# Kernel optimization log

Measured on AMD Instinct MI355X. Metric: run time of the kernel, lower is better.

## Reference

```python
import jax, jax.numpy as jnp
import numpy as np

SCALE = 2
GROUPS = 4

def _up_axis(x, axis, s):
    # torch F.interpolate bilinear, align_corners=False, along one axis
    n = x.shape[axis]
    src = jnp.maximum((jnp.arange(n * s, dtype=jnp.float32) + 0.5) / s - 0.5, 0.0)
    i0 = jnp.minimum(jnp.floor(src).astype(jnp.int32), n - 1)
    i1 = jnp.minimum(i0 + 1, n - 1)
    t = (src - i0.astype(jnp.float32)).astype(x.dtype)
    shp = [1] * x.ndim
    shp[axis] = -1
    t = t.reshape(shp)
    return jnp.take(x, i0, axis=axis) * (1 - t) + jnp.take(x, i1, axis=axis) * t

def _grid_sample(img, grid):
    # img: (N,C,H,W); grid: (N,Hg,Wg,2) xy in [-1,1]; bilinear, align_corners=False, zeros padding
    N, C, H, W = img.shape
    gx = (grid[..., 0] + 1.0) * (W * 0.5) - 0.5
    gy = (grid[..., 1] + 1.0) * (H * 0.5) - 0.5
    x0 = jnp.floor(gx)
    y0 = jnp.floor(gy)
    tx = (gx - x0).astype(img.dtype)
    ty = (gy - y0).astype(img.dtype)
    x0 = x0.astype(jnp.int32)
    y0 = y0.astype(jnp.int32)
    flat = img.reshape(N, C, H * W)

    def corner(xi, yi, wgt):
        valid = ((xi >= 0) & (xi < W) & (yi >= 0) & (yi < H)).astype(img.dtype)
        idx = (jnp.clip(yi, 0, H - 1) * W + jnp.clip(xi, 0, W - 1)).reshape(N, -1)
        v = jax.vmap(lambda f, i: f[:, i])(flat, idx)  # (N,C,P) irregular gather
        return v * (wgt * valid).reshape(N, 1, -1)

    out = (corner(x0, y0, (1 - tx) * (1 - ty))
           + corner(x0 + 1, y0, tx * (1 - ty))
           + corner(x0, y0 + 1, (1 - tx) * ty)
           + corner(x0 + 1, y0 + 1, tx * ty))
    return out.reshape(N, C, grid.shape[1], grid.shape[2])

def _forward(x, w_off, b_off, w_mask, b_mask):
    s, g = SCALE, GROUPS
    b, c, h, w = x.shape
    # 1x1 convs
    offset = jnp.einsum('bchw,oc->bohw', x, w_off) + b_off[None, :, None, None]  # (b,2g,h,w)
    mask = jax.nn.sigmoid(jnp.einsum('bchw,gc->bghw', x, w_mask) + b_mask[None, :, None, None])  # (b,g,h,w)
    # bilinear upsample then split into s*s subpixel feature maps (one per group)
    x_up = _up_axis(_up_axis(x, 2, s), 3, s)  # (b,c,s*h,s*w)
    feat = x_up.reshape(b, c, s, h, s, w).transpose(0, 2, 4, 1, 3, 5).reshape(b, s * s, c, h, w)[:, :g]
    # per-group offset-perturbed sampling coordinates
    off = offset.reshape(b, g, 2, h, w).transpose(0, 1, 3, 4, 2)  # (b,g,h,w,2) (x,y)
    gy, gx = jnp.meshgrid(jnp.arange(h, dtype=x.dtype), jnp.arange(w, dtype=x.dtype), indexing='ij')
    base = jnp.stack([gx, gy], axis=-1)  # (h,w,2)
    coords = base[None, None] + off
    norm = (coords / jnp.array([w, h], dtype=x.dtype) - 0.5) * 2.0
    sampled = _grid_sample(feat.reshape(b * g, c, h, w), norm.reshape(b * g, h, w, 2))
    sampled = sampled.reshape(b, g, c, h, w)
    # sigmoid-mask weighting and group-sum reduction
    return (sampled * mask[:, :, None]).sum(axis=1)  # (b,c,h,w)

def setup_inputs():
    key = jax.random.key(0)
    k1, k2, k3, k4, k5 = jax.random.split(key, 5)
    b, c, h, w, g = 16, 64, 128, 128, GROUPS
    return {
        'x': jax.random.normal(k1, (b, c, h, w), jnp.float32),
        'w_off': jax.random.normal(k2, (2 * g, c), jnp.float32) * 0.1,
        'b_off': jax.random.normal(k3, (2 * g,), jnp.float32) * 0.1,
        'w_mask': jax.random.normal(k4, (g, c), jnp.float32) * 0.1,
        'b_mask': jax.random.normal(k5, (g,), jnp.float32) * 0.1,
    }

def reference(x, w_off, b_off, w_mask, b_mask):
    return _forward(x, w_off, b_off, w_mask, b_mask)
```

## Files before the change

kernel.cpp:

```cpp
#include <hip/hip_runtime.h>
#include <hip/hip_fp16.h>

#define CC 64
#define HH 128
#define WW 128
#define HWS (HH * WW)
#define NG 4

__device__ __forceinline__ void make_taps(float gp, int n, int half, int& base,
                                          float& w0o, float& w1o, float& w2o) {
  float w0 = 0.0f, w1 = 0.0f, w2 = 0.0f;
  float f = floorf(gp);
  int x0 = (int)f;
  float t = gp - f;
  int b = 0;
#pragma unroll
  for (int k = 0; k < 2; ++k) {
    int xc = x0 + k;
    float cw = k ? t : 1.0f - t;
    if (xc < 0 || xc >= n) cw = 0.0f;
    int xcc = min(max(xc, 0), n - 1);
    int u = half * n + xcc;
    float src = fmaxf((float)u * 0.5f - 0.25f, 0.0f);
    float sf = floorf(src);
    int i0 = (int)sf;
    float tu = src - sf;
    int i1 = min(i0 + 1, n - 1);
    if (k == 0) b = i0;
    int s0 = i0 - b;
    int s1 = i1 - b;
    float a0 = cw * (1.0f - tu);
    float a1 = cw * tu;
    w0 += (s0 == 0) ? a0 : 0.0f;
    w1 += (s0 == 1) ? a0 : 0.0f;
    w0 += (s1 == 0) ? a1 : 0.0f;
    w1 += (s1 == 1) ? a1 : 0.0f;
    w2 += (s1 == 2) ? a1 : 0.0f;
  }
  base = b;
  w0o = w0; w1o = w1; w2o = w2;
}

__global__ __launch_bounds__(256) void prep_v3(
    const float* __restrict__ x,
    const float* __restrict__ w_off, const float* __restrict__ b_off,
    const float* __restrict__ w_mask, const float* __restrict__ b_mask,
    __half* __restrict__ xT, float* __restrict__ geomC, int npix) {
  __shared__ float wt[CC * 12];
  __shared__ unsigned int tile[64][33];
  __shared__ float part[4][64][13];
  int t = threadIdx.x;
  for (int idx = t; idx < CC * 12; idx += 256) {
    int c = idx / 12, d = idx - c * 12;
    wt[idx] = (d < 8) ? w_off[d * CC + c] : w_mask[(d - 8) * CC + c];
  }
  __syncthreads();

  int px = t & 63, chq = t >> 6;
  int pix = blockIdx.x * 64 + px;
  int b = pix >> 14;
  int ij = pix & (HWS - 1);
  const float* __restrict__ xp = x + (size_t)b * CC * HWS + ij;

  float xv[16];
#pragma unroll
  for (int k = 0; k < 16; ++k) xv[k] = xp[(size_t)(chq * 16 + k) * HWS];

  float p12[12];
#pragma unroll
  for (int d = 0; d < 12; ++d) p12[d] = 0.0f;
#pragma unroll
  for (int k = 0; k < 16; ++k) {
    int c = chq * 16 + k;
    float v = xv[k];
    const float4 w0 = *reinterpret_cast<const float4*>(&wt[c * 12 + 0]);
    const float4 w1 = *reinterpret_cast<const float4*>(&wt[c * 12 + 4]);
    const float4 w2 = *reinterpret_cast<const float4*>(&wt[c * 12 + 8]);
    p12[0]  = fmaf(w0.x, v, p12[0]);   p12[1]  = fmaf(w0.y, v, p12[1]);
    p12[2]  = fmaf(w0.z, v, p12[2]);   p12[3]  = fmaf(w0.w, v, p12[3]);
    p12[4]  = fmaf(w1.x, v, p12[4]);   p12[5]  = fmaf(w1.y, v, p12[5]);
    p12[6]  = fmaf(w1.z, v, p12[6]);   p12[7]  = fmaf(w1.w, v, p12[7]);
    p12[8]  = fmaf(w2.x, v, p12[8]);   p12[9]  = fmaf(w2.y, v, p12[9]);
    p12[10] = fmaf(w2.z, v, p12[10]);  p12[11] = fmaf(w2.w, v, p12[11]);
  }

#pragma unroll
  for (int k = 0; k < 8; ++k) {
    tile[px][chq * 8 + k] = __builtin_bit_cast(
        unsigned int, __floats2half2_rn(xv[2 * k], xv[2 * k + 1]));
  }
#pragma unroll
  for (int d = 0; d < 12; ++d) part[chq][px][d] = p12[d];
  __syncthreads();

  {
    unsigned int* __restrict__ xtu = reinterpret_cast<unsigned int*>(xT);
    size_t base = (size_t)blockIdx.x * 64 * 32;
    int spx = t >> 2, c0 = (t & 3) * 8;
    uint4 u0, u1;
    u0.x = tile[spx][c0 + 0]; u0.y = tile[spx][c0 + 1];
    u0.z = tile[spx][c0 + 2]; u0.w = tile[spx][c0 + 3];
    u1.x = tile[spx][c0 + 4]; u1.y = tile[spx][c0 + 5];
    u1.z = tile[spx][c0 + 6]; u1.w = tile[spx][c0 + 7];
    *reinterpret_cast<uint4*>(xtu + base + t * 8) = u0;
    *reinterpret_cast<uint4*>(xtu + base + t * 8 + 4) = u1;
  }

  if (t < 64) {
    int pixg = blockIdx.x * 64 + t;
    int ijg = pixg & (HWS - 1);
    int i = ijg >> 7, j = ijg & (WW - 1);
    float a12[12];
#pragma unroll
    for (int d = 0; d < 12; ++d) {
      a12[d] = ((d < 8) ? b_off[d] : b_mask[d - 8]) + part[0][t][d] +
               part[1][t][d] + part[2][t][d] + part[3][t][d];
    }
    float* __restrict__ gb = geomC + (size_t)(pixg >> 5) * 1024 + (pixg & 31);
#pragma unroll
    for (int g = 0; g < NG; ++g) {
      int sy = g >> 1, sx = g & 1;
      float mg = 1.0f / (1.0f + __expf(-a12[8 + g]));
      int cb, rb;
      float x0, x1, x2, y0, y1, y2;
      make_taps((float)j + a12[2 * g]     - 0.5f, WW, sx, cb, x0, x1, x2);
      make_taps((float)i + a12[2 * g + 1] - 0.5f, HH, sy, rb, y0, y1, y2);
      gb[(g * 8 + 0) * 32] = x0;
      gb[(g * 8 + 1) * 32] = x1;
      gb[(g * 8 + 2) * 32] = x2;
      gb[(g * 8 + 3) * 32] = y0 * mg;
      gb[(g * 8 + 4) * 32] = y1 * mg;
      gb[(g * 8 + 5) * 32] = y2 * mg;
      gb[(g * 8 + 6) * 32] = __int_as_float(rb);
      gb[(g * 8 + 7) * 32] = __int_as_float(cb);
    }
  }
}

__global__ __launch_bounds__(256) void sample16(
    const __half* __restrict__ xT, const float* __restrict__ geomC,
    float* __restrict__ out, int npix) {
  __shared__ float graw[1024];
  __shared__ int2 gexp[32][36];
  int t = threadIdx.x;

  int nwg = gridDim.x, bid = blockIdx.x;
  int swz = ((nwg & 7) == 0) ? ((bid & 7) * (nwg >> 3) + (bid >> 3)) : bid;

  int b  = swz >> 9;
  int w_ = swz & 511;
  int ty = w_ >> 4, tx = w_ & 15;
  int i0 = ty * 4, j0 = tx * 8;

  {
    int tr = t >> 6, d = (t & 63) >> 1, q = t & 1;
    int grp = (b << 9) + (i0 + tr) * 4 + (j0 >> 5);
    const uint4 v = *reinterpret_cast<const uint4*>(
        geomC + (size_t)grp * 1024 + d * 32 + (j0 & 31) + q * 4);
    *reinterpret_cast<uint4*>(&graw[tr * 256 + d * 8 + q * 4]) = v;
  }
  __syncthreads();

  if (t < 128) {
    int p = t >> 2, g = t & 3;
    int base = (p >> 3) * 256 + (p & 7);
    float wx0 = graw[base + (g * 8 + 0) * 8];
    float wx1 = graw[base + (g * 8 + 1) * 8];
    float wx2 = graw[base + (g * 8 + 2) * 8];
    float wy0 = graw[base + (g * 8 + 3) * 8];
    float wy1 = graw[base + (g * 8 + 4) * 8];
    float wy2 = graw[base + (g * 8 + 5) * 8];
    int rb = __float_as_int(graw[base + (g * 8 + 6) * 8]);
    int cb = __float_as_int(graw[base + (g * 8 + 7) * 8]);
#pragma unroll
    for (int dy = 0; dy < 3; ++dy) {
      int ro = min(rb + dy, HH - 1) * WW;
      float wyv = (dy == 0) ? wy0 : ((dy == 1) ? wy1 : wy2);
#pragma unroll
      for (int dx = 0; dx < 3; ++dx) {
        int off = ro + min(cb + dx, WW - 1);
        float wv = wyv * ((dx == 0) ? wx0 : ((dx == 1) ? wx1 : wx2));
        gexp[p][g * 9 + dy * 3 + dx] =
            make_int2(off, __builtin_bit_cast(int, __float2half2_rn(wv)));
      }
    }
  }
  __syncthreads();

  int p = t >> 3, r = t & 7;
  int tr = p >> 3, pc = p & 7;
  int ij = (i0 + tr) * WW + (j0 + pc);
  const __half* __restrict__ xb = xT + ((size_t)b * HWS) * 64 + r * 8;

  __half2 acc0 = __float2half2_rn(0.0f);
  __half2 acc1 = acc0, acc2 = acc0, acc3 = acc0;

#pragma unroll
  for (int k0 = 0; k0 < 36; k0 += 9) {
    __half2 wh[9];
    int off[9];
#pragma unroll
    for (int k = 0; k < 9; ++k) {
      int2 ow = gexp[p][k0 + k];
      off[k] = ow.x;
      wh[k] = __builtin_bit_cast(__half2, ow.y);
    }
    uint4 v[9];
#pragma unroll
    for (int k = 0; k < 9; ++k) {
      v[k] = *reinterpret_cast<const uint4*>(xb + (size_t)off[k] * 64);
    }
    asm volatile("" ::
        "v"(v[0].x), "v"(v[1].x), "v"(v[2].x),
        "v"(v[3].x), "v"(v[4].x), "v"(v[5].x),
        "v"(v[6].x), "v"(v[7].x), "v"(v[8].x));
#pragma unroll
    for (int k = 0; k < 9; ++k) {
      acc0 = __hfma2(__builtin_bit_cast(__half2, v[k].x), wh[k], acc0);
      acc1 = __hfma2(__builtin_bit_cast(__half2, v[k].y), wh[k], acc1);
      acc2 = __hfma2(__builtin_bit_cast(__half2, v[k].z), wh[k], acc2);
      acc3 = __hfma2(__builtin_bit_cast(__half2, v[k].w), wh[k], acc3);
    }
  }

  float2 f0 = __half22float2(acc0);
  float2 f1 = __half22float2(acc1);
  float2 f2 = __half22float2(acc2);
  float2 f3 = __half22float2(acc3);
  float* __restrict__ op = out + ((size_t)b * CC + r * 8) * HWS + ij;
  op[0 * HWS] = f0.x;  op[1 * HWS] = f0.y;
  op[2 * HWS] = f1.x;  op[3 * HWS] = f1.y;
  op[4 * HWS] = f2.x;  op[5 * HWS] = f2.y;
  op[6 * HWS] = f3.x;  op[7 * HWS] = f3.y;
}

__global__ __launch_bounds__(256) void dysample_fused(
    const float* __restrict__ x,
    const float* __restrict__ w_off, const float* __restrict__ b_off,
    const float* __restrict__ w_mask, const float* __restrict__ b_mask,
    float* __restrict__ out, int npix) {
  __shared__ float wt[CC * 12];
  for (int idx = threadIdx.x; idx < CC * 12; idx += 256) {
    int c = idx / 12, d = idx - c * 12;
    wt[idx] = (d < 8) ? w_off[d * CC + c] : w_mask[(d - 8) * CC + c];
  }
  __syncthreads();
  int nwg = gridDim.x;
  int bid = blockIdx.x;
  int swz = ((nwg & 7) == 0) ? ((bid & 7) * (nwg >> 3) + (bid >> 3)) : bid;
  int pix = swz * 256 + threadIdx.x;
  if (pix >= npix) return;
  int b = pix >> 14;
  int ij = pix & (HWS - 1);
  int i = ij >> 7, j = ij & (WW - 1);
  const float* __restrict__ xp = x + (size_t)b * CC * HWS;
  float a12[12];
#pragma unroll
  for (int d = 0; d < 12; ++d) a12[d] = (d < 8) ? b_off[d] : b_mask[d - 8];
#pragma unroll 4
  for (int c = 0; c < CC; ++c) {
    float xv = xp[c * HWS + ij];
    const float4 w0 = *reinterpret_cast<const float4*>(&wt[c * 12 + 0]);
    const float4 w1 = *reinterpret_cast<const float4*>(&wt[c * 12 + 4]);
    const float4 w2 = *reinterpret_cast<const float4*>(&wt[c * 12 + 8]);
    a12[0]  = fmaf(w0.x, xv, a12[0]);   a12[1]  = fmaf(w0.y, xv, a12[1]);
    a12[2]  = fmaf(w0.z, xv, a12[2]);   a12[3]  = fmaf(w0.w, xv, a12[3]);
    a12[4]  = fmaf(w1.x, xv, a12[4]);   a12[5]  = fmaf(w1.y, xv, a12[5]);
    a12[6]  = fmaf(w1.z, xv, a12[6]);   a12[7]  = fmaf(w1.w, xv, a12[7]);
    a12[8]  = fmaf(w2.x, xv, a12[8]);   a12[9]  = fmaf(w2.y, xv, a12[9]);
    a12[10] = fmaf(w2.z, xv, a12[10]);  a12[11] = fmaf(w2.w, xv, a12[11]);
  }
  int ro[NG][3], co[NG][3];
  float wx[NG][3], wy[NG][3];
#pragma unroll
  for (int g = 0; g < NG; ++g) {
    int sy = g >> 1, sx = g & 1;
    float mg = 1.0f / (1.0f + __expf(-a12[8 + g]));
    int cb, rb;
    float x0, x1, x2, y0, y1, y2;
    make_taps((float)j + a12[2 * g]     - 0.5f, WW, sx, cb, x0, x1, x2);
    make_taps((float)i + a12[2 * g + 1] - 0.5f, HH, sy, rb, y0, y1, y2);
    wx[g][0] = x0;      wx[g][1] = x1;      wx[g][2] = x2;
    wy[g][0] = y0 * mg; wy[g][1] = y1 * mg; wy[g][2] = y2 * mg;
#pragma unroll
    for (int d = 0; d < 3; ++d) {
      ro[g][d] = min(rb + d, HH - 1) * WW;
      co[g][d] = min(cb + d, WW - 1);
    }
  }
  float* __restrict__ op = out + (size_t)b * CC * HWS + ij;
  for (int blk = 0; blk < 4; ++blk) {
    const float* __restrict__ xb = xp + blk * 16 * HWS;
    float acc[16];
#pragma unroll
    for (int c = 0; c < 16; ++c) acc[c] = 0.0f;
#pragma unroll
    for (int g = 0; g < NG; ++g) {
      int o9[9];
      float w9[9];
#pragma unroll
      for (int dy = 0; dy < 3; ++dy) {
#pragma unroll
        for (int dx = 0; dx < 3; ++dx) {
          o9[dy * 3 + dx] = ro[g][dy] + co[g][dx];
          w9[dy * 3 + dx] = wy[g][dy] * wx[g][dx];
        }
      }
#pragma unroll
      for (int c = 0; c < 16; ++c) {
        const float* __restrict__ xc = xb + c * HWS;
#pragma unroll
        for (int k = 0; k < 9; ++k) acc[c] = fmaf(w9[k], xc[o9[k]], acc[c]);
      }
    }
#pragma unroll
    for (int c = 0; c < 16; ++c) op[(blk * 16 + c) * HWS] = acc[c];
  }
}

extern "C" void kernel_launch(void* const* d_in, const int* in_sizes, int n_in,
                              void* d_out, int out_size, void* d_ws, size_t ws_size,
                              hipStream_t stream) {
  const float* x      = (const float*)d_in[0];
  const float* w_off  = (const float*)d_in[1];
  const float* b_off  = (const float*)d_in[2];
  const float* w_mask = (const float*)d_in[3];
  const float* b_mask = (const float*)d_in[4];
  float* out = (float*)d_out;

  int B = in_sizes[0] / (CC * HWS);
  int npix = B * HWS;
  size_t need = (size_t)npix * 128 + (size_t)npix * 128;

  if (ws_size >= need && (npix & (HWS - 1)) == 0) {
    __half* xT   = (__half*)d_ws;
    float* geomC = (float*)((char*)d_ws + (size_t)npix * 128);
    hipLaunchKernelGGL(prep_v3, dim3(npix / 64), dim3(256), 0, stream,
                       x, w_off, b_off, w_mask, b_mask, xT, geomC, npix);
    hipLaunchKernelGGL(sample16, dim3(npix / 32), dim3(256), 0, stream,
                       xT, geomC, out, npix);
  } else {
    int nblk = (npix + 255) / 256;
    hipLaunchKernelGGL(dysample_fused, dim3(nblk), dim3(256), 0, stream,
                       x, w_off, b_off, w_mask, b_mask, out, npix);
  }
}
```

Baseline: 83.66 us.

## Stage per-group source windows in LDS and gather taps from shared memory

The sampling kernel now cooperatively loads, per block, an 8x10 pixel window of the fp16 channel-last source for each of the four groups into a swizzled LDS buffer. Each 3x3 tap whose location falls inside the window is read from LDS, and taps outside it fall back to a global gather, with the branch encoded in the sign of the offset. The aim is to replace many scattered, overlapping global gathers with one coalesced prefetch plus LDS reads. The cost is extra LDS use (40KB), a divergent per-tap branch, and loss of the batched 9-load memory-level parallelism in the tap loop.

```diff
diff --git a/kernel.cpp b/kernel.cpp
--- a/kernel.cpp
+++ b/kernel.cpp
@@ -6,6 +6,9 @@
 #define WW 128
 #define HWS (HH * WW)
 #define NG 4
+#define NR 8
+#define NC 10
+#define NLINE (NG * NR * NC)
 
 __device__ __forceinline__ void make_taps(float gp, int n, int half, int& base,
                                           float& w0o, float& w1o, float& w2o) {
@@ -41,6 +44,15 @@
   w0o = w0; w1o = w1; w2o = w2;
 }
 
+__device__ __forceinline__ int winR0(int g, int i0) {
+  int sy = g >> 1;
+  return min(max(64 * sy + ((i0 - 3) >> 1) - 1, 0), HH - NR);
+}
+__device__ __forceinline__ int winC0(int g, int j0) {
+  int sx = g & 1;
+  return min(max(64 * sx + ((j0 - 3) >> 1) - 1, 0), WW - NC);
+}
+
 __global__ __launch_bounds__(256) void prep_v3(
     const float* __restrict__ x,
     const float* __restrict__ w_off, const float* __restrict__ b_off,
@@ -142,6 +154,7 @@
     float* __restrict__ out, int npix) {
   __shared__ float graw[1024];
   __shared__ int2 gexp[32][36];
+  __shared__ __align__(16) char win[NLINE * 128];
   int t = threadIdx.x;
 
   int nwg = gridDim.x, bid = blockIdx.x;
@@ -151,6 +164,8 @@
   int w_ = swz & 511;
   int ty = w_ >> 4, tx = w_ & 15;
   int i0 = ty * 4, j0 = tx * 8;
+
+  const __half* __restrict__ xbase = xT + ((size_t)b * HWS) * 64;
 
   {
     int tr = t >> 6, d = (t & 63) >> 1, q = t & 1;
@@ -158,6 +173,19 @@
     const uint4 v = *reinterpret_cast<const uint4*>(
         geomC + (size_t)grp * 1024 + d * 32 + (j0 & 31) + q * 4);
     *reinterpret_cast<uint4*>(&graw[tr * 256 + d * 8 + q * 4]) = v;
+  }
+
+#pragma unroll
+  for (int m = 0; m < 10; ++m) {
+    int l = m * 32 + (t >> 3);
+    int q = t & 7;
+    int g = l / 80;
+    int rem = l - g * 80;
+    int rr = rem / 10, cc = rem - rr * 10;
+    int sp = (winR0(g, i0) + rr) * WW + (winC0(g, j0) + cc);
+    uint4 v = *reinterpret_cast<const uint4*>(xbase + (size_t)sp * 64 + q * 8);
+    *reinterpret_cast<uint4*>(
+        win + l * 128 + ((q * 16) ^ ((l & 7) << 4))) = v;
   }
   __syncthreads();
 
@@ -172,16 +200,23 @@
     float wy2 = graw[base + (g * 8 + 5) * 8];
     int rb = __float_as_int(graw[base + (g * 8 + 6) * 8]);
     int cb = __float_as_int(graw[base + (g * 8 + 7) * 8]);
+    int R0 = winR0(g, i0), C0 = winC0(g, j0);
 #pragma unroll
     for (int dy = 0; dy < 3; ++dy) {
-      int ro = min(rb + dy, HH - 1) * WW;
+      int row = min(rb + dy, HH - 1);
       float wyv = (dy == 0) ? wy0 : ((dy == 1) ? wy1 : wy2);
 #pragma unroll
       for (int dx = 0; dx < 3; ++dx) {
-        int off = ro + min(cb + dx, WW - 1);
+        int col = min(cb + dx, WW - 1);
         float wv = wyv * ((dx == 0) ? wx0 : ((dx == 1) ? wx1 : wx2));
+        int rr = row - R0, cc = col - C0;
+        int e;
+        if (rr >= 0 && rr < NR && cc >= 0 && cc < NC)
+          e = (g * (NR * NC) + rr * NC + cc) * 128;
+        else
+          e = -(row * WW + col) - 1;
         gexp[p][g * 9 + dy * 3 + dx] =
-            make_int2(off, __builtin_bit_cast(int, __float2half2_rn(wv)));
+            make_int2(e, __builtin_bit_cast(int, __float2half2_rn(wv)));
       }
     }
   }
@@ -190,37 +225,27 @@
   int p = t >> 3, r = t & 7;
   int tr = p >> 3, pc = p & 7;
   int ij = (i0 + tr) * WW + (j0 + pc);
-  const __half* __restrict__ xb = xT + ((size_t)b * HWS) * 64 + r * 8;
+  const __half* __restrict__ xb = xbase + r * 8;
+  int rsw = r * 16;
 
   __half2 acc0 = __float2half2_rn(0.0f);
   __half2 acc1 = acc0, acc2 = acc0, acc3 = acc0;
 
 #pragma unroll
-  for (int k0 = 0; k0 < 36; k0 += 9) {
-    __half2 wh[9];
-    int off[9];
-#pragma unroll
-    for (int k = 0; k < 9; ++k) {
-      int2 ow = gexp[p][k0 + k];
-      off[k] = ow.x;
-      wh[k] = __builtin_bit_cast(__half2, ow.y);
-    }
-    uint4 v[9];
-#pragma unroll
-    for (int k = 0; k < 9; ++k) {
-      v[k] = *reinterpret_cast<const uint4*>(xb + (size_t)off[k] * 64);
-    }
-    asm volatile("" ::
-        "v"(v[0].x), "v"(v[1].x), "v"(v[2].x),
-        "v"(v[3].x), "v"(v[4].x), "v"(v[5].x),
-        "v"(v[6].x), "v"(v[7].x), "v"(v[8].x));
-#pragma unroll
-    for (int k = 0; k < 9; ++k) {
-      acc0 = __hfma2(__builtin_bit_cast(__half2, v[k].x), wh[k], acc0);
-      acc1 = __hfma2(__builtin_bit_cast(__half2, v[k].y), wh[k], acc1);
-      acc2 = __hfma2(__builtin_bit_cast(__half2, v[k].z), wh[k], acc2);
-      acc3 = __hfma2(__builtin_bit_cast(__half2, v[k].w), wh[k], acc3);
-    }
+  for (int k = 0; k < 36; ++k) {
+    int2 ow = gexp[p][k];
+    __half2 wh = __builtin_bit_cast(__half2, ow.y);
+    uint4 v;
+    if (ow.x >= 0) {
+      int la = ow.x + (rsw ^ ((ow.x >> 3) & 0x70));
+      v = *reinterpret_cast<const uint4*>(win + la);
+    } else {
+      v = *reinterpret_cast<const uint4*>(xb + (size_t)(-ow.x - 1) * 64);
+    }
+    acc0 = __hfma2(__builtin_bit_cast(__half2, v.x), wh, acc0);
+    acc1 = __hfma2(__builtin_bit_cast(__half2, v.y), wh, acc1);
+    acc2 = __hfma2(__builtin_bit_cast(__half2, v.z), wh, acc2);
+    acc3 = __hfma2(__builtin_bit_cast(__half2, v.w), wh, acc3);
   }
 
   float2 f0 = __half22float2(acc0);
```

New measurement: 116.8 us. 1.4x slower.
